# Kernel optimization log

Hardware: AMD Instinct MI355X
Metric: run time of the kernel (lower is better)

The kernel has to match this reference:

```python
import jax, jax.numpy as jnp
import numpy as np

B = 1_000_000
N_DIR, N_TRIAL = 2, 4
ALPHA, R_GAS, EPS = 0.3, 8.314462618, 1e-12
TAU_CLIP, LN_CLIP = 10.0, 20.0
EPS_FD, SIGMA, MARGIN = 1e-4, 0.05, 0.0
LAM_PHY, LAM_GD, LAM_TPD = 1.0, 0.1, 0.1


def renorm3(x):
    # clamp to >=0 and normalize so components sum to 1 (last axis)
    x = jnp.maximum(x, 0.0)
    return x / jnp.maximum(x.sum(-1, keepdims=True), EPS)


def nrtl_ln_gamma(x, T, g):
    # x: (B,3), T: (B,), g: (B,3,3) -> ln_gamma: (B,3)
    x = jnp.maximum(x, 0.0)
    Tc = jnp.maximum(T, 1.0)
    tau = jnp.clip(g / (R_GAS * jnp.maximum(Tc, EPS)[:, None, None]), -TAU_CLIP, TAU_CLIP)
    G = jnp.exp(-ALPHA * tau)
    denom = jnp.maximum(jnp.einsum('bj,bji->bi', x, G), EPS)          # (B,3)
    A = jnp.einsum('bj,bji->bi', x, tau * G)                          # (B,3), == num1 in torch
    term1 = A / denom
    W = x[:, None, :] * G / denom[:, None, :]                         # (B,3,3)
    inside = tau - (A / denom)[:, None, :]
    term2 = (W * inside).sum(-1)
    return jnp.clip(term1 + term2, -LN_CLIP, LN_CLIP)


def setup_inputs() -> dict:
    key = jax.random.key(0)
    k1, k2, k3, k4, k5, k6 = jax.random.split(key, 6)
    pred = jax.random.uniform(k1, (B, 6), dtype=jnp.float32, minval=0.01, maxval=1.0)
    target = jax.random.uniform(k2, (B, 6), dtype=jnp.float32, minval=0.01, maxval=1.0)
    T = 298.0 + 100.0 * jax.random.uniform(k3, (B,), dtype=jnp.float32)  # Kelvin
    g = 800.0 * jax.random.normal(k4, (B, 3, 3), dtype=jnp.float32)      # J/mol
    # simplex directions: zero-sum, unit-norm (matches _sample_simplex_directions)
    v = jax.random.normal(k5, (N_DIR, B, 3), dtype=jnp.float32)
    v = v - v.mean(-1, keepdims=True)
    dirs = v / jnp.maximum(jnp.linalg.norm(v, axis=-1, keepdims=True), 1e-12)
    noise = SIGMA * jax.random.normal(k6, (N_TRIAL, B, 3), dtype=jnp.float32)
    return {'pred': pred, 'target': target, 'T': T, 'g': g, 'dirs': dirs, 'noise': noise}


def reference(pred, target, T, g, dirs, noise):
    # supervised MSE on (E+R) compositions
    L_sup = jnp.mean((pred - target) ** 2)

    xE = renorm3(pred[:, :3])
    xR = renorm3(pred[:, 3:])
    ln_gE = nrtl_ln_gamma(xE, T, g)
    ln_gR = nrtl_ln_gamma(xR, T, g)
    # chemical potential residual r_k = ln(xE_k gE_k) - ln(xR_k gR_k)
    r = jnp.log(jnp.maximum(xE, EPS)) + ln_gE - (jnp.log(jnp.maximum(xR, EPS)) + ln_gR)
    L_phy = jnp.mean(r ** 2)

    lg = jax.vmap(lambda xx: nrtl_ln_gamma(xx, T, g))  # over trial/direction axis

    # Gibbs-Duhem finite-difference penalty along simplex directions
    x_p = renorm3(xE[None] + EPS_FD * dirs)            # (N_DIR,B,3)
    x_m = renorm3(xE[None] - EPS_FD * dirs)
    d_ln = (lg(x_p) - lg(x_m)) / (2.0 * EPS_FD)
    gd = (xE[None] * d_ln).sum(-1)                     # (N_DIR,B)
    L_gd = jnp.mean(gd * gd)

    # TPD stability penalty
    w = renorm3(xE[None] + noise)                      # (N_TRIAL,B,3)
    ln_gw = lg(w)
    tpd = (w * (jnp.log(jnp.maximum(w, EPS)) + ln_gw
                - jnp.log(jnp.maximum(xE, EPS))[None] - ln_gE[None])).sum(-1)
    L_tpd = jnp.mean(jnp.maximum(MARGIN - tpd, 0.0))

    return L_sup + LAM_PHY * L_phy + LAM_GD * L_gd + LAM_TPD * L_tpd
```

## Files before the change

kernel.cpp:

```cpp
#include <hip/hip_runtime.h>


constexpr float ALPHA    = 0.3f;
constexpr float R_GAS    = 8.314462618f;
constexpr float EPS      = 1e-12f;
constexpr float TAU_CLIP = 10.0f;
constexpr float LN_CLIP  = 20.0f;
constexpr float EPS_FD   = 1e-4f;

constexpr float LOG2E = 1.44269504088896340736f;
constexpr float LN2   = 0.69314718055994530942f;

__device__ __forceinline__ float clipf(float v, float lo, float hi) {
    return fminf(fmaxf(v, lo), hi);
}
__device__ __forceinline__ float fast_rcp(float x) { return __builtin_amdgcn_rcpf(x); }

struct Mats {
    float tau[3][3];
    float G[3][3];
    float tG[3][3];
};

__device__ __forceinline__ void ln_gamma3(const float x[3], const Mats& M, float lg[3]) {
    float ratio[3], invd[3];
#pragma unroll
    for (int i = 0; i < 3; ++i) {
        float d = x[0] * M.G[0][i] + x[1] * M.G[1][i] + x[2] * M.G[2][i];
        d = fmaxf(d, EPS);
        float A = x[0] * M.tG[0][i] + x[1] * M.tG[1][i] + x[2] * M.tG[2][i];
        float inv = fast_rcp(d);
        invd[i] = inv;
        ratio[i] = A * inv;
    }
#pragma unroll
    for (int i = 0; i < 3; ++i) {
        float s = ratio[i];
#pragma unroll
        for (int j = 0; j < 3; ++j) {
            s += x[j] * M.G[i][j] * invd[j] * (M.tau[i][j] - ratio[j]);
        }
        lg[i] = clipf(s, -LN_CLIP, LN_CLIP);
    }
}

__device__ __forceinline__ void renorm3(float x[3]) {
    x[0] = fmaxf(x[0], 0.0f);
    x[1] = fmaxf(x[1], 0.0f);
    x[2] = fmaxf(x[2], 0.0f);
    float inv = fast_rcp(fmaxf(x[0] + x[1] + x[2], EPS));
    x[0] *= inv; x[1] *= inv; x[2] *= inv;
}

__global__ __launch_bounds__(256) void nrtl_loss_kernel(
    const float* __restrict__ pred,
    const float* __restrict__ target,
    const float* __restrict__ Tarr,
    const float* __restrict__ g,
    const float* __restrict__ dirs,
    const float* __restrict__ noise,
    float* __restrict__ partials, int B)
{
    __shared__ __align__(16) float sh[8448];
    float* s_pred  = sh;
    float* s_g     = sh + 1536;
    float* s_dirs  = sh + 3840;
    float* s_noise = sh + 5376;

    const int t  = threadIdx.x;
    const int s0 = blockIdx.x * 256;
    const int ns = min(256, B - s0);

    const float invB  = 1.0f / (float)B;
    const float SUP_W = invB * (1.0f / 6.0f);
    const float PHY_W = invB * (1.0f / 3.0f);
    const float GD_W  = invB * 0.1f * 0.5f;
    const float TPD_W = invB * 0.1f * 0.25f;

    float contrib = 0.0f;

    if (ns == 256) {
        const float4* pg4 = (const float4*)(pred   + (size_t)s0 * 6);
        const float4* tg4 = (const float4*)(target + (size_t)s0 * 6);
        const float4* gg4 = (const float4*)(g      + (size_t)s0 * 9);
        float4* sp4 = (float4*)s_pred;
        float4* sg4 = (float4*)s_g;

        {
            float4 pa = pg4[t], ta = tg4[t];
            sp4[t] = pa;
            float dx = pa.x - ta.x, dy = pa.y - ta.y, dz = pa.z - ta.z, dw = pa.w - ta.w;
            contrib += SUP_W * (dx * dx + dy * dy + dz * dz + dw * dw);
            if (t < 128) {
                float4 pb = pg4[256 + t], tb = tg4[256 + t];
                sp4[256 + t] = pb;
                float ex = pb.x - tb.x, ey = pb.y - tb.y, ez = pb.z - tb.z, ew = pb.w - tb.w;
                contrib += SUP_W * (ex * ex + ey * ey + ez * ez + ew * ew);
            }
        }
        sg4[t]       = gg4[t];
        sg4[256 + t] = gg4[256 + t];
        if (t < 64) sg4[512 + t] = gg4[512 + t];
#pragma unroll
        for (int d = 0; d < 2; ++d)
            if (t < 192)
                ((float4*)(s_dirs + d * 768))[t] =
                    ((const float4*)(dirs + ((size_t)d * B + s0) * 3))[t];
#pragma unroll
        for (int tr = 0; tr < 4; ++tr)
            if (t < 192)
                ((float4*)(s_noise + tr * 768))[t] =
                    ((const float4*)(noise + ((size_t)tr * B + s0) * 3))[t];
    } else {
        const float* pg = pred   + (size_t)s0 * 6;
        const float* tg = target + (size_t)s0 * 6;
        for (int j = t; j < ns * 6; j += 256) {
            float pv = pg[j], tv = tg[j];
            s_pred[j] = pv;
            float d = pv - tv;
            contrib += SUP_W * d * d;
        }
        const float* gg = g + (size_t)s0 * 9;
        for (int j = t; j < ns * 9; j += 256) s_g[j] = gg[j];
        for (int d = 0; d < 2; ++d) {
            const float* dg = dirs + ((size_t)d * B + s0) * 3;
            for (int j = t; j < ns * 3; j += 256) s_dirs[d * 768 + j] = dg[j];
        }
        for (int tr = 0; tr < 4; ++tr) {
            const float* ng = noise + ((size_t)tr * B + s0) * 3;
            for (int j = t; j < ns * 3; j += 256) s_noise[tr * 768 + j] = ng[j];
        }
    }
    __syncthreads();

    if (t < ns) {
        float xE[3] = {s_pred[t * 6],     s_pred[t * 6 + 1], s_pred[t * 6 + 2]};
        float xR[3] = {s_pred[t * 6 + 3], s_pred[t * 6 + 4], s_pred[t * 6 + 5]};
        renorm3(xE);
        renorm3(xR);

        const float Tc = fmaxf(Tarr[s0 + t], 1.0f);
        const float invRT = fast_rcp(R_GAS * Tc);
        Mats M;
#pragma unroll
        for (int a = 0; a < 3; ++a) {
#pragma unroll
            for (int b = 0; b < 3; ++b) {
                float ta = clipf(s_g[t * 9 + a * 3 + b] * invRT, -TAU_CLIP, TAU_CLIP);
                float Gv = __builtin_amdgcn_exp2f((-ALPHA * LOG2E) * ta);
                M.tau[a][b] = ta;
                M.G[a][b]   = Gv;
                M.tG[a][b]  = ta * Gv;
            }
        }

        float lgE[3], lgR[3];
        ln_gamma3(xE, M, lgE);
        ln_gamma3(xR, M, lgR);

        float logxE[3];
        float phy = 0.0f;
#pragma unroll
        for (int k = 0; k < 3; ++k) {
            logxE[k] = LN2 * __builtin_amdgcn_logf(fmaxf(xE[k], EPS));
            float logxR = LN2 * __builtin_amdgcn_logf(fmaxf(xR[k], EPS));
            float r = logxE[k] + lgE[k] - logxR - lgR[k];
            phy += r * r;
        }
        contrib += PHY_W * phy;

        float gdsum = 0.0f;
#pragma unroll
        for (int d = 0; d < 2; ++d) {
            float xp[3], xm[3];
#pragma unroll
            for (int k = 0; k < 3; ++k) {
                float dvk = s_dirs[d * 768 + t * 3 + k];
                xp[k] = xE[k] + EPS_FD * dvk;
                xm[k] = xE[k] - EPS_FD * dvk;
            }
            renorm3(xp);
            renorm3(xm);
            float lgp[3], lgm[3];
            ln_gamma3(xp, M, lgp);
            ln_gamma3(xm, M, lgm);
            float gd = 0.0f;
            const float inv2e = 0.5f / EPS_FD;
#pragma unroll
            for (int k = 0; k < 3; ++k) gd += xE[k] * ((lgp[k] - lgm[k]) * inv2e);
            gdsum += gd * gd;
        }
        contrib += GD_W * gdsum;

        float tpdsum = 0.0f;
#pragma unroll
        for (int tr = 0; tr < 4; ++tr) {
            float w[3];
#pragma unroll
            for (int k = 0; k < 3; ++k) w[k] = xE[k] + s_noise[tr * 768 + t * 3 + k];
            renorm3(w);
            float lgw[3];
            ln_gamma3(w, M, lgw);
            float tpd = 0.0f;
#pragma unroll
            for (int k = 0; k < 3; ++k) {
                float logw = LN2 * __builtin_amdgcn_logf(fmaxf(w[k], EPS));
                tpd += w[k] * (logw + lgw[k] - logxE[k] - lgE[k]);
            }
            tpdsum += fmaxf(-tpd, 0.0f);
        }
        contrib += TPD_W * tpdsum;
    }

#pragma unroll
    for (int off = 32; off > 0; off >>= 1)
        contrib += __shfl_down(contrib, off, 64);

    __shared__ float ssum[4];
    const int lane = threadIdx.x & 63;
    const int wid  = threadIdx.x >> 6;
    if (lane == 0) ssum[wid] = contrib;
    __syncthreads();
    if (threadIdx.x == 0) {
        partials[blockIdx.x] = ssum[0] + ssum[1] + ssum[2] + ssum[3];
    }
}

__global__ __launch_bounds__(256) void reduce_kernel(
    const float* __restrict__ partials, int n, float* __restrict__ out)
{
    double sacc = 0.0;
    for (int j = threadIdx.x; j < n; j += 256) sacc += (double)partials[j];
#pragma unroll
    for (int off = 32; off > 0; off >>= 1)
        sacc += __shfl_down(sacc, off, 64);
    __shared__ double ds[4];
    const int lane = threadIdx.x & 63;
    const int wid  = threadIdx.x >> 6;
    if (lane == 0) ds[wid] = sacc;
    __syncthreads();
    if (threadIdx.x == 0) out[0] = (float)(ds[0] + ds[1] + ds[2] + ds[3]);
}

extern "C" void kernel_launch(void* const* d_in, const int* in_sizes, int n_in,
                              void* d_out, int out_size, void* d_ws, size_t ws_size,
                              hipStream_t stream) {
    const float* pred   = (const float*)d_in[0];
    const float* target = (const float*)d_in[1];
    const float* Tarr   = (const float*)d_in[2];
    const float* g      = (const float*)d_in[3];
    const float* dirs   = (const float*)d_in[4];
    const float* noise  = (const float*)d_in[5];
    const int B = in_sizes[2];

    float* partials = (float*)d_ws;
    float* out      = (float*)d_out;

    const int block = 256;
    const int grid  = (B + block - 1) / block;
    nrtl_loss_kernel<<<grid, block, 0, stream>>>(pred, target, Tarr, g, dirs, noise, partials, B);
    reduce_kernel<<<1, block, 0, stream>>>(partials, grid, out);
}
```

Before: 192.9 us.

## Stage block inputs into LDS via direct global_load_lds DMA

Replaces the register-staged float4 copies into shared memory with __builtin_amdgcn_global_load_lds transfers spread round-robin across the four waves. Target and T are now also staged in LDS, and the supervised MSE is computed per sample from LDS rather than during the load. The intent is to skip the VGPR round trip and cut load-issue instructions in a memory-bound kernel. In exchange, LDS use per block grows, which may lower occupancy, and the code depends on the direct-to-LDS load builtin with 16-byte width being supported on this target.

```diff
diff --git a/kernel.cpp b/kernel.cpp
--- a/kernel.cpp
+++ b/kernel.cpp
@@ -61,15 +61,74 @@
     const float* __restrict__ noise,
     float* __restrict__ partials, int B)
 {
-    __shared__ __align__(16) float sh[8448];
+    __shared__ __align__(16) float sh[10240];
     float* s_pred  = sh;
-    float* s_g     = sh + 1536;
-    float* s_dirs  = sh + 3840;
-    float* s_noise = sh + 5376;
-
-    const int t  = threadIdx.x;
-    const int s0 = blockIdx.x * 256;
-    const int ns = min(256, B - s0);
+    float* s_targ  = sh + 1536;
+    float* s_g     = sh + 3072;
+    float* s_dirs  = sh + 5376;
+    float* s_noise = sh + 6912;
+    float* s_T     = sh + 9984;
+
+    const int t    = threadIdx.x;
+    const int wid  = t >> 6;
+    const int lane = t & 63;
+    const int s0   = blockIdx.x * 256;
+    const int ns   = min(256, B - s0);
+
+    if (ns == 256) {
+        const float* pb = pred   + (size_t)s0 * 6;
+        const float* tb = target + (size_t)s0 * 6;
+        const float* gb = g      + (size_t)s0 * 9;
+        const float* d0 = dirs  + ((size_t)0 * B + s0) * 3;
+        const float* d1 = dirs  + ((size_t)1 * B + s0) * 3;
+        const float* n0 = noise + ((size_t)0 * B + s0) * 3;
+        const float* n1 = noise + ((size_t)1 * B + s0) * 3;
+        const float* n2 = noise + ((size_t)2 * B + s0) * 3;
+        const float* n3 = noise + ((size_t)3 * B + s0) * 3;
+        const float* Tb = Tarr + s0;
+
+        auto dma = [&](const float* src, int loff) {
+            __builtin_amdgcn_global_load_lds(
+                (const __attribute__((address_space(1))) unsigned int*)(src + lane * 4),
+                (__attribute__((address_space(3))) unsigned int*)(sh + loff),
+                16, 0, 0);
+        };
+#pragma unroll
+        for (int k = 0; k < 6; ++k)  if (((0  + k) & 3) == wid) dma(pb + k * 256, 0    + k * 256);
+#pragma unroll
+        for (int k = 0; k < 6; ++k)  if (((6  + k) & 3) == wid) dma(tb + k * 256, 1536 + k * 256);
+#pragma unroll
+        for (int k = 0; k < 9; ++k)  if (((12 + k) & 3) == wid) dma(gb + k * 256, 3072 + k * 256);
+#pragma unroll
+        for (int k = 0; k < 3; ++k)  if (((21 + k) & 3) == wid) dma(d0 + k * 256, 5376 + k * 256);
+#pragma unroll
+        for (int k = 0; k < 3; ++k)  if (((24 + k) & 3) == wid) dma(d1 + k * 256, 6144 + k * 256);
+#pragma unroll
+        for (int k = 0; k < 3; ++k)  if (((27 + k) & 3) == wid) dma(n0 + k * 256, 6912 + k * 256);
+#pragma unroll
+        for (int k = 0; k < 3; ++k)  if (((30 + k) & 3) == wid) dma(n1 + k * 256, 7680 + k * 256);
+#pragma unroll
+        for (int k = 0; k < 3; ++k)  if (((33 + k) & 3) == wid) dma(n2 + k * 256, 8448 + k * 256);
+#pragma unroll
+        for (int k = 0; k < 3; ++k)  if (((36 + k) & 3) == wid) dma(n3 + k * 256, 9216 + k * 256);
+        if ((39 & 3) == wid) dma(Tb, 9984);
+    } else {
+        const float* pb = pred   + (size_t)s0 * 6;
+        const float* tb = target + (size_t)s0 * 6;
+        const float* gb = g      + (size_t)s0 * 9;
+        for (int j = t; j < ns * 6; j += 256) { s_pred[j] = pb[j]; s_targ[j] = tb[j]; }
+        for (int j = t; j < ns * 9; j += 256) s_g[j] = gb[j];
+        for (int d = 0; d < 2; ++d) {
+            const float* dg = dirs + ((size_t)d * B + s0) * 3;
+            for (int j = t; j < ns * 3; j += 256) s_dirs[d * 768 + j] = dg[j];
+        }
+        for (int tr = 0; tr < 4; ++tr) {
+            const float* ng = noise + ((size_t)tr * B + s0) * 3;
+            for (int j = t; j < ns * 3; j += 256) s_noise[tr * 768 + j] = ng[j];
+        }
+        for (int j = t; j < ns; j += 256) s_T[j] = Tarr[s0 + j];
+    }
+    __syncthreads();
 
     const float invB  = 1.0f / (float)B;
     const float SUP_W = invB * (1.0f / 6.0f);
@@ -79,67 +138,21 @@
 
     float contrib = 0.0f;
 
-    if (ns == 256) {
-        const float4* pg4 = (const float4*)(pred   + (size_t)s0 * 6);
-        const float4* tg4 = (const float4*)(target + (size_t)s0 * 6);
-        const float4* gg4 = (const float4*)(g      + (size_t)s0 * 9);
-        float4* sp4 = (float4*)s_pred;
-        float4* sg4 = (float4*)s_g;
-
-        {
-            float4 pa = pg4[t], ta = tg4[t];
-            sp4[t] = pa;
-            float dx = pa.x - ta.x, dy = pa.y - ta.y, dz = pa.z - ta.z, dw = pa.w - ta.w;
-            contrib += SUP_W * (dx * dx + dy * dy + dz * dz + dw * dw);
-            if (t < 128) {
-                float4 pb = pg4[256 + t], tb = tg4[256 + t];
-                sp4[256 + t] = pb;
-                float ex = pb.x - tb.x, ey = pb.y - tb.y, ez = pb.z - tb.z, ew = pb.w - tb.w;
-                contrib += SUP_W * (ex * ex + ey * ey + ez * ez + ew * ew);
-            }
-        }
-        sg4[t]       = gg4[t];
-        sg4[256 + t] = gg4[256 + t];
-        if (t < 64) sg4[512 + t] = gg4[512 + t];
-#pragma unroll
-        for (int d = 0; d < 2; ++d)
-            if (t < 192)
-                ((float4*)(s_dirs + d * 768))[t] =
-                    ((const float4*)(dirs + ((size_t)d * B + s0) * 3))[t];
-#pragma unroll
-        for (int tr = 0; tr < 4; ++tr)
-            if (t < 192)
-                ((float4*)(s_noise + tr * 768))[t] =
-                    ((const float4*)(noise + ((size_t)tr * B + s0) * 3))[t];
-    } else {
-        const float* pg = pred   + (size_t)s0 * 6;
-        const float* tg = target + (size_t)s0 * 6;
-        for (int j = t; j < ns * 6; j += 256) {
-            float pv = pg[j], tv = tg[j];
-            s_pred[j] = pv;
-            float d = pv - tv;
-            contrib += SUP_W * d * d;
-        }
-        const float* gg = g + (size_t)s0 * 9;
-        for (int j = t; j < ns * 9; j += 256) s_g[j] = gg[j];
-        for (int d = 0; d < 2; ++d) {
-            const float* dg = dirs + ((size_t)d * B + s0) * 3;
-            for (int j = t; j < ns * 3; j += 256) s_dirs[d * 768 + j] = dg[j];
-        }
-        for (int tr = 0; tr < 4; ++tr) {
-            const float* ng = noise + ((size_t)tr * B + s0) * 3;
-            for (int j = t; j < ns * 3; j += 256) s_noise[tr * 768 + j] = ng[j];
-        }
-    }
-    __syncthreads();
-
     if (t < ns) {
-        float xE[3] = {s_pred[t * 6],     s_pred[t * 6 + 1], s_pred[t * 6 + 2]};
-        float xR[3] = {s_pred[t * 6 + 3], s_pred[t * 6 + 4], s_pred[t * 6 + 5]};
+        float p6[6], t6[6];
+#pragma unroll
+        for (int k = 0; k < 6; ++k) { p6[k] = s_pred[t * 6 + k]; t6[k] = s_targ[t * 6 + k]; }
+        float sup = 0.0f;
+#pragma unroll
+        for (int k = 0; k < 6; ++k) { float d = p6[k] - t6[k]; sup += d * d; }
+        contrib += SUP_W * sup;
+
+        float xE[3] = {p6[0], p6[1], p6[2]};
+        float xR[3] = {p6[3], p6[4], p6[5]};
         renorm3(xE);
         renorm3(xR);
 
-        const float Tc = fmaxf(Tarr[s0 + t], 1.0f);
+        const float Tc = fmaxf(s_T[t], 1.0f);
         const float invRT = fast_rcp(R_GAS * Tc);
         Mats M;
 #pragma unroll
@@ -217,13 +230,9 @@
         contrib += __shfl_down(contrib, off, 64);
 
     __shared__ float ssum[4];
-    const int lane = threadIdx.x & 63;
-    const int wid  = threadIdx.x >> 6;
     if (lane == 0) ssum[wid] = contrib;
     __syncthreads();
-    if (threadIdx.x == 0) {
-        partials[blockIdx.x] = ssum[0] + ssum[1] + ssum[2] + ssum[3];
-    }
+    if (t == 0) partials[blockIdx.x] = ssum[0] + ssum[1] + ssum[2] + ssum[3];
 }
 
 __global__ __launch_bounds__(256) void reduce_kernel(
```

Result: faster. 182.5 us (-5.4%).
